# Optimization experiments

Hardware: AMD Instinct MI355X
Metric: run time of the kernel (lower is better)

## Reference

```python
import jax, jax.numpy as jnp
import numpy as np

N, B, PER, NELEM, E = 8192, 32, 256, 5, 131072
H, F, G, L = 128, 128, 50, 6
NC = B * NELEM
CUTOFF = 10.0
LOG2 = float(np.log(2.0))


def ssp(x):
    return jax.nn.softplus(x) - LOG2


def setup_inputs() -> dict:
    key = jax.random.key(0)
    ks = jax.random.split(key, 24)
    pos = jax.random.normal(ks[0], (N, 3), dtype=jnp.float32) * 2.0
    # component structure: node n in graph g gets element slot n % NELEM
    comp_id = (jnp.arange(N) // PER) * NELEM + (jnp.arange(N) % NELEM)
    comps_z = jax.random.randint(ks[1], (NC,), 1, 100)
    z = comps_z[comp_id]
    # edges restricted to within a graph (mimics radius_graph with batch)
    eg = jax.random.randint(ks[2], (E,), 0, B)
    src = eg * PER + jax.random.randint(ks[3], (E,), 0, PER)
    dst = eg * PER + jax.random.randint(ks[4], (E,), 0, PER)
    edge_index = jnp.stack([src, dst], axis=0)
    s = 0.05
    p = lambda k, shp: jax.random.normal(k, shp, dtype=jnp.float32) * s
    return {
        "pos": pos,
        "emb_table": p(ks[5], (100, H)),
        "mlp_w1": p(ks[6], (L, G, F)),
        "mlp_b1": jnp.zeros((L, F), jnp.float32),
        "mlp_w2": p(ks[7], (L, F, F)),
        "mlp_b2": jnp.zeros((L, F), jnp.float32),
        "cf_lin1_w": p(ks[8], (L, H, F)),
        "cf_lin2_w": p(ks[9], (L, F, H)),
        "cf_lin2_b": jnp.zeros((L, H), jnp.float32),
        "int_lin_w": p(ks[10], (L, H, H)),
        "int_lin_b": jnp.zeros((L, H), jnp.float32),
        "out_w1": p(ks[11], (H, H // 2)),
        "out_b1": jnp.zeros((H // 2,), jnp.float32),
        "out_w2": p(ks[12], (H // 2, 1)),
        "out_b2": jnp.zeros((1,), jnp.float32),
        "z": z,
        "comp_id": comp_id,
        "edge_index": edge_index,
        "comps_z": comps_z,
    }


def reference(pos, emb_table, mlp_w1, mlp_b1, mlp_w2, mlp_b2,
              cf_lin1_w, cf_lin2_w, cf_lin2_b, int_lin_w, int_lin_b,
              out_w1, out_b1, out_w2, out_b2,
              z, comp_id, edge_index, comps_z):
    src, dst = edge_index[0], edge_index[1]
    # edge distances and Gaussian smearing
    ew = jnp.linalg.norm(pos[src] - pos[dst], axis=-1)              # [E]
    offset = jnp.linspace(0.0, CUTOFF, G)
    coeff = -0.5 / (offset[1] - offset[0]) ** 2
    edge_attr = jnp.exp(coeff * (ew[:, None] - offset[None, :]) ** 2)  # [E,G]
    # cutoff envelope used by CFConv
    C = CUTOFF / (1e-10 + ew ** 2) - 1.0                            # [E]

    h = emb_table[z]                 # [N,H] node features (fixed across blocks)
    types = emb_table[comps_z]       # [NC,H] component features

    counts = jax.ops.segment_sum(jnp.ones((N,), jnp.float32), comp_id,
                                 num_segments=NC)                   # [NC]
    batch_c = jnp.arange(NC) // NELEM

    for i in range(L):
        # edge filter MLP * cutoff weight
        W = ssp(edge_attr @ mlp_w1[i] + mlp_b1[i]) @ mlp_w2[i] + mlp_b2[i]
        W = W * C[:, None]                                          # [E,F]
        xh = h @ cf_lin1_w[i]                                       # [N,F]
        msg = xh[src] * W                                           # [E,F]
        agg = jax.ops.segment_sum(msg, dst, num_segments=N)         # [N,F]
        # per-component mean pooling
        comp = jax.ops.segment_sum(agg, comp_id, num_segments=NC) / counts[:, None]
        x = comp @ cf_lin2_w[i] + cf_lin2_b[i]                      # [NC,H]
        x = ssp(x) @ int_lin_w[i] + int_lin_b[i]
        types = types + x

    # readout (num_tasks=1, n_seq=None branch)
    h2 = ssp(types @ out_w1 + out_b1)
    per_comp = h2 @ out_w2 + out_b2                                 # [NC,1]
    out = jax.ops.segment_sum(per_comp, batch_c, num_segments=B)    # [B,1]
    return out
```

## Files before the change

kernel.cpp:

```cpp
#include <hip/hip_runtime.h>


#define NNODES 8192
#define NGRAPH 32
#define NELEM  5
#define NEDGE  131072
#define HD     128
#define FD     128
#define GD     50
#define LL     6
#define NC     160
#define NZ     100
#define CUT    10.0f
#define LOG2_  0.69314718055994531f
#define LOG2E_ 1.44269504088896340f
#define QDC    0.84932181f

#define CAP    1024
#define PADE   (NC * CAP)
#define PADG   (PADE / 64)
#define GPITCH 72
#define TPITCH 136
#define CSTR   16

#define W1F_ELEMS (LL * 2 * 8 * 64 * 8)
#define W2F_ELEMS (LL * 4 * 8 * 64 * 8)
#define NSCATB   (NEDGE / 256)
#define NFRAGB   ((W1F_ELEMS + W2F_ELEMS) / 256)
#define NXHZB    (LL * NZ / 2)
#define NB2PB    3

typedef _Float16 half8 __attribute__((ext_vector_type(8)));
typedef float floatx4 __attribute__((ext_vector_type(4)));

#if __has_builtin(__builtin_amdgcn_exp2f)
#define EXP2F(x) __builtin_amdgcn_exp2f(x)
#else
#define EXP2F(x) __expf((x) * LOG2_)
#endif
#if __has_builtin(__builtin_amdgcn_logf)
#define LOG2F_(x) __builtin_amdgcn_logf(x)
#else
#define LOG2F_(x) (__logf(x) * LOG2E_)
#endif

__device__ __forceinline__ float ssp(float x) {
    float m = fmaxf(x, 0.0f);
    float z = __expf(-fabsf(x));
    return m + __logf(1.0f + z) - LOG2_;
}

__global__ __launch_bounds__(256) void setup_kernel(
    const float* __restrict__ pos, const int* __restrict__ ei,
    const int* __restrict__ comp_id, const int* __restrict__ z,
    const float* __restrict__ w1, const float* __restrict__ w2,
    const float* __restrict__ b2in,
    const float* __restrict__ emb, const float* __restrict__ cf1,
    int* __restrict__ counts, int* __restrict__ cursor,
    float* __restrict__ ew_s, float* __restrict__ c_s, int* __restrict__ zsrc_s,
    _Float16* __restrict__ w1f, _Float16* __restrict__ w2f,
    float* __restrict__ xh_z, float* __restrict__ b2p)
{
    int bx = blockIdx.x;
    int tid = threadIdx.x;
    if (bx < NSCATB) {
        int e = bx * 256 + tid;
        int s = ei[e], d = ei[NEDGE + e];
        float dx = pos[3*s]   - pos[3*d];
        float dy = pos[3*s+1] - pos[3*d+1];
        float dz = pos[3*s+2] - pos[3*d+2];
        float d2 = dx*dx + dy*dy + dz*dz;
        float ew = sqrtf(d2);
        float C  = CUT / (1e-10f + d2) - 1.0f;
        int cid = comp_id[d];
        int idx = cid * CAP + atomicAdd(&cursor[cid * CSTR], 1);
        ew_s[idx] = ew; c_s[idx] = C; zsrc_s[idx] = z[s];
        if (e < NNODES) atomicAdd(&counts[comp_id[e]], 1);
        return;
    }
    int fx = bx - NSCATB;
    if (fx < NFRAGB) {
        int idx = fx * 256 + tid;
        if (idx < W1F_ELEMS) {
            int j = idx & 7, lane = (idx >> 3) & 63, tcg = (idx >> 9) & 7;
            int kb = (idx >> 12) & 1, l = idx >> 13;
            int k = kb * 32 + (lane >> 4) * 8 + j;
            int col = tcg * 16 + (lane & 15);
            float v = (k < GD) ? w1[(l * GD + k) * FD + col] : 0.0f;
            w1f[idx] = (_Float16)(v * LOG2E_);
        } else {
            int id2 = idx - W1F_ELEMS;
            int j = id2 & 7, lane = (id2 >> 3) & 63, tcg = (id2 >> 9) & 7;
            int kb = (id2 >> 12) & 3, l = id2 >> 14;
            int k = kb * 32 + (lane >> 4) * 8 + j;
            int col = tcg * 16 + (lane & 15);
            w2f[id2] = (_Float16)(LOG2_ * w2[(l * FD + k) * FD + col]);
        }
        return;
    }
    int bz = fx - NFRAGB;
    if (bz < NXHZB) {
        int l = bz / (NZ / 2);
        int zv = (bz % (NZ / 2)) * 2 + (tid >> 7);
        int f = tid & 127;
        const float* h = emb + zv * HD;
        const float* w = cf1 + l * HD * FD;
        float acc = 0.0f;
        #pragma unroll 8
        for (int k = 0; k < HD; ++k) acc = fmaf(h[k], w[k * FD + f], acc);
        int fp = ((f >> 5) * 32) + ((f & 15) * 2) + ((f >> 4) & 1);
        xh_z[(l * NZ + zv) * FD + fp] = acc;
    } else {
        int idx2 = (bz - NXHZB) * 256 + tid;
        int l = idx2 >> 7, fo = idx2 & 127;
        float sum = 0.0f;
        #pragma unroll 8
        for (int fi = 0; fi < FD; ++fi)
            sum += (float)(_Float16)(LOG2_ * w2[(l * FD + fi) * FD + fo]);
        b2p[idx2] = b2in[l * FD + fo] - sum;
    }
}

__global__ __launch_bounds__(256, 6) void edge_kernel(
    const float* __restrict__ ew_s, const float* __restrict__ c_s,
    const int* __restrict__ zsrc_s,
    const _Float16* __restrict__ w1f, const float* __restrict__ b1_,
    const _Float16* __restrict__ w2f, const float* __restrict__ b2p_,
    const float* __restrict__ xh_z, float* __restrict__ comp_acc)
{
    __shared__ __align__(16) _Float16 smem[64 * TPITCH];
    __shared__ int2 cz_l[64];

    const int tid  = threadIdx.x;
    const int lane = tid & 63;
    const int l15  = lane & 15;
    const int quad = lane >> 4;
    const int fq   = __builtin_amdgcn_readfirstlane(tid >> 6);
    const int cid  = blockIdx.x % NC;
    const int gg   = blockIdx.x / NC;
    const int g0   = cid * CAP + gg * 64;
    const int l0   = blockIdx.y * 3;

    const float ce = c_s[g0 + lane];
    if (__all(ce == 0.0f)) return;
    if (tid < 64)
        cz_l[tid] = make_int2(__float_as_int(ce), zsrc_s[g0 + tid] * (FD * 4));

    const float delta = CUT / (GD - 1);
    const float Qe = QDC / delta;
    half8 ga, gb;
    {
        const float qewr = ew_s[g0 + lane] * Qe;
        #pragma unroll
        for (int i = 0; i < 8; ++i) {
            float u0 = qewr - (fq * 16 + i) * QDC;
            float u1 = qewr - (fq * 16 + 8 + i) * QDC;
            ga[i] = (_Float16)EXP2F(-(u0 * u0));
            gb[i] = (_Float16)EXP2F(-(u1 * u1));
        }
    }
    const int colbase = fq * 32 + l15;
    const int wsw = quad << 4;
    const int rsw = ((l15 >> 2) & 3) << 4;

    #pragma unroll 1
    for (int li = 0; li < 3; ++li) {
        const int l = l0 + li;

        *(half8*)&smem[lane * GPITCH + fq * 16]     = ga;
        *(half8*)&smem[lane * GPITCH + fq * 16 + 8] = gb;
        const float b1c0 = b1_[l * FD + colbase] * LOG2E_;
        const float b1c1 = b1_[l * FD + colbase + 16] * LOG2E_;
        const float b2c0 = b2p_[l * FD + colbase];
        const float b2c1 = b2p_[l * FD + colbase + 16];
        __syncthreads();

        floatx4 accT[4][2];
        #pragma unroll
        for (int tr = 0; tr < 4; ++tr) {
            accT[tr][0] = (floatx4){b1c0, b1c0, b1c0, b1c0};
            accT[tr][1] = (floatx4){b1c1, b1c1, b1c1, b1c1};
        }
        const half8* w1fp = (const half8*)w1f;
        #pragma unroll
        for (int kb = 0; kb < 2; ++kb) {
            half8 bf0 = w1fp[((l * 2 + kb) * 8 + fq * 2 + 0) * 64 + lane];
            half8 bf1 = w1fp[((l * 2 + kb) * 8 + fq * 2 + 1) * 64 + lane];
            #pragma unroll
            for (int tr = 0; tr < 4; ++tr) {
                half8 af = *(const half8*)&smem[(tr * 16 + l15) * GPITCH + kb * 32 + quad * 8];
                accT[tr][0] = __builtin_amdgcn_mfma_f32_16x16x32_f16(af, bf0, accT[tr][0], 0, 0, 0);
                accT[tr][1] = __builtin_amdgcn_mfma_f32_16x16x32_f16(af, bf1, accT[tr][1], 0, 0, 0);
            }
        }
        __syncthreads();

        #pragma unroll
        for (int tr = 0; tr < 4; ++tr) {
            #pragma unroll
            for (int tcl = 0; tcl < 2; ++tcl) {
                #pragma unroll
                for (int r = 0; r < 4; ++r) {
                    float ee = EXP2F(accT[tr][tcl][r]);
                    smem[(tr * 16 + quad * 4 + r) * TPITCH
                         + ((fq * 32 + tcl * 16 + l15) ^ wsw)]
                        = (_Float16)LOG2F_(1.0f + ee);
                }
            }
        }
        __syncthreads();

        floatx4 accW[4][2];
        #pragma unroll
        for (int tr = 0; tr < 4; ++tr) {
            accW[tr][0] = (floatx4){b2c0, b2c0, b2c0, b2c0};
            accW[tr][1] = (floatx4){b2c1, b2c1, b2c1, b2c1};
        }
        const half8* w2fp = (const half8*)w2f;
        #pragma unroll
        for (int kb = 0; kb < 4; ++kb) {
            half8 bf0 = w2fp[((l * 4 + kb) * 8 + fq * 2 + 0) * 64 + lane];
            half8 bf1 = w2fp[((l * 4 + kb) * 8 + fq * 2 + 1) * 64 + lane];
            #pragma unroll
            for (int tr = 0; tr < 4; ++tr) {
                half8 af = *(const half8*)&smem[(tr * 16 + l15) * TPITCH
                                                + ((kb * 32 + quad * 8) ^ rsw)];
                accW[tr][0] = __builtin_amdgcn_mfma_f32_16x16x32_f16(af, bf0, accW[tr][0], 0, 0, 0);
                accW[tr][1] = __builtin_amdgcn_mfma_f32_16x16x32_f16(af, bf1, accW[tr][1], 0, 0, 0);
            }
        }

        const char* xb = (const char*)xh_z
                       + ((size_t)(l * NZ * FD) + (size_t)(fq * 32 + l15 * 2)) * 4;
        float s0 = 0.0f, s1 = 0.0f;
        #pragma unroll
        for (int tr = 0; tr < 4; ++tr) {
            #pragma unroll
            for (int r = 0; r < 4; ++r) {
                const int e = tr * 16 + quad * 4 + r;
                int2 cz = cz_l[e];
                float cee = __int_as_float(cz.x);
                const float2 xr = *(const float2*)(xb + cz.y);
                s0 = fmaf(accW[tr][0][r], cee * xr.x, s0);
                s1 = fmaf(accW[tr][1][r], cee * xr.y, s1);
            }
        }
        s0 += __shfl_xor(s0, 16); s0 += __shfl_xor(s0, 32);
        s1 += __shfl_xor(s1, 16); s1 += __shfl_xor(s1, 32);
        float* cacc = comp_acc + (l * NC + cid) * FD + fq * 32;
        if (quad == 0) {
            atomicAdd(&cacc[l15],      s0);
            atomicAdd(&cacc[l15 + 16], s1);
        }
        if (li < 2) __syncthreads();
    }
}

__global__ __launch_bounds__(128) void comp_kernel(
    const float* __restrict__ comp_acc, const int* __restrict__ counts,
    const float* __restrict__ cf2w, const float* __restrict__ cf2b,
    const float* __restrict__ intw, const float* __restrict__ intb,
    float* __restrict__ types_acc)
{
    int c = blockIdx.x, l = blockIdx.y, f = threadIdx.x;
    __shared__ float comp[FD];
    __shared__ float sx[FD];
    comp[f] = comp_acc[(l * NC + c) * FD + f] / (float)counts[c];
    __syncthreads();
    float acc = cf2b[l * HD + f];
    const float* w = cf2w + l * FD * HD;
    #pragma unroll 8
    for (int k = 0; k < FD; ++k) acc = fmaf(comp[k], w[k * HD + f], acc);
    sx[f] = ssp(acc);
    __syncthreads();
    float acc2 = intb[l * HD + f];
    const float* wi = intw + l * HD * HD;
    #pragma unroll 8
    for (int k = 0; k < HD; ++k) acc2 = fmaf(sx[k], wi[k * HD + f], acc2);
    atomicAdd(&types_acc[c * HD + f], acc2);
}

__global__ __launch_bounds__(64) void readout_kernel(
    const float* __restrict__ types_acc, const float* __restrict__ emb,
    const int* __restrict__ comps_z,
    const float* __restrict__ w1, const float* __restrict__ b1,
    const float* __restrict__ w2, const float* __restrict__ b2,
    float* __restrict__ out)
{
    int b = blockIdx.x, lane = threadIdx.x;
    float sum = 0.0f;
    for (int cc = 0; cc < NELEM; ++cc) {
        int c = b * NELEM + cc;
        int zc = comps_z[c];
        float acc = b1[lane];
        const float* ta = types_acc + c * HD;
        const float* eb = emb + zc * HD;
        #pragma unroll 8
        for (int k = 0; k < HD; ++k) acc = fmaf(ta[k] + eb[k], w1[k * 64 + lane], acc);
        sum += ssp(acc) * w2[lane];
    }
    #pragma unroll
    for (int s = 32; s > 0; s >>= 1) sum += __shfl_xor(sum, s);
    if (lane == 0) out[b] = sum + (float)NELEM * b2[0];
}

extern "C" void kernel_launch(void* const* d_in, const int* in_sizes, int n_in,
                              void* d_out, int out_size, void* d_ws, size_t ws_size,
                              hipStream_t stream) {
    (void)in_sizes; (void)n_in; (void)out_size; (void)ws_size;
    const float* pos     = (const float*)d_in[0];
    const float* emb     = (const float*)d_in[1];
    const float* mlp_w1  = (const float*)d_in[2];
    const float* mlp_b1  = (const float*)d_in[3];
    const float* mlp_w2  = (const float*)d_in[4];
    const float* mlp_b2  = (const float*)d_in[5];
    const float* cf1     = (const float*)d_in[6];
    const float* cf2w    = (const float*)d_in[7];
    const float* cf2b    = (const float*)d_in[8];
    const float* intw    = (const float*)d_in[9];
    const float* intb    = (const float*)d_in[10];
    const float* ow1     = (const float*)d_in[11];
    const float* ob1     = (const float*)d_in[12];
    const float* ow2     = (const float*)d_in[13];
    const float* ob2     = (const float*)d_in[14];
    const int*   z       = (const int*)d_in[15];
    const int*   comp_id = (const int*)d_in[16];
    const int*   ei      = (const int*)d_in[17];
    const int*   comps_z = (const int*)d_in[18];
    float* out = (float*)d_out;

    char* ws = (char*)d_ws;
    size_t off = 0;
    auto alloc = [&](size_t bytes) -> void* {
        void* p = ws + off;
        off += (bytes + 255) & ~(size_t)255;
        return p;
    };
    float* comp_acc  = (float*)alloc((size_t)LL * NC * FD * 4);
    int*   counts    = (int*)  alloc(NC * 4);
    float* types_acc = (float*)alloc((size_t)NC * HD * 4);
    int*   cursor    = (int*)  alloc(NC * CSTR * 4);
    float* c_s       = (float*)alloc((size_t)PADE * 4);
    int*   zsrc_s    = (int*)  alloc((size_t)PADE * 4);
    float* ew_s      = (float*)alloc((size_t)PADE * 4);
    size_t zero_bytes = off;
    float* xh_z     = (float*)alloc((size_t)LL * NZ * FD * 4);
    float* b2p      = (float*)alloc((size_t)LL * FD * 4);
    _Float16* w1f   = (_Float16*)alloc((size_t)W1F_ELEMS * 2);
    _Float16* w2f   = (_Float16*)alloc((size_t)W2F_ELEMS * 2);

    hipMemsetAsync(d_ws, 0, zero_bytes, stream);

    setup_kernel<<<NSCATB + NFRAGB + NXHZB + NB2PB, 256, 0, stream>>>(
        pos, ei, comp_id, z, mlp_w1, mlp_w2, mlp_b2, emb, cf1,
        counts, cursor, ew_s, c_s, zsrc_s, w1f, w2f, xh_z, b2p);
    edge_kernel <<<dim3(PADG, 2), 256, 0, stream>>>(ew_s, c_s, zsrc_s,
                                                    w1f, mlp_b1, w2f, b2p,
                                                    xh_z, comp_acc);
    comp_kernel <<<dim3(NC, LL), 128, 0, stream>>>(comp_acc, counts, cf2w, cf2b,
                                                   intw, intb, types_acc);
    readout_kernel<<<NGRAPH, 64, 0, stream>>>(types_acc, emb, comps_z,
                                              ow1, ob1, ow2, ob2, out);
}
```

Before: 224.7 us.

## Launch one edge block per layer and pack softplus writes with permuted W2 fragments

Result: faster. 214.8 us (-4.4%).

```diff
diff --git a/kernel.cpp b/kernel.cpp
--- a/kernel.cpp
+++ b/kernel.cpp
@@ -31,6 +31,7 @@
 #define NB2PB    3
 
 typedef _Float16 half8 __attribute__((ext_vector_type(8)));
+typedef __fp16 fp16x2 __attribute__((ext_vector_type(2)));
 typedef float floatx4 __attribute__((ext_vector_type(4)));
 
 #if __has_builtin(__builtin_amdgcn_exp2f)
@@ -92,7 +93,8 @@
             int id2 = idx - W1F_ELEMS;
             int j = id2 & 7, lane = (id2 >> 3) & 63, tcg = (id2 >> 9) & 7;
             int kb = (id2 >> 12) & 3, l = id2 >> 14;
-            int k = kb * 32 + (lane >> 4) * 8 + j;
+            int kf = (lane >> 4) * 8 + j;
+            int k = kb * 32 + ((kf & 1) << 4) + (kf >> 1);
             int col = tcg * 16 + (lane & 15);
             w2f[id2] = (_Float16)(LOG2_ * w2[(l * FD + k) * FD + col]);
         }
@@ -121,7 +123,7 @@
     }
 }
 
-__global__ __launch_bounds__(256, 6) void edge_kernel(
+__global__ __launch_bounds__(256, 8) void edge_kernel(
     const float* __restrict__ ew_s, const float* __restrict__ c_s,
     const int* __restrict__ zsrc_s,
     const _Float16* __restrict__ w1f, const float* __restrict__ b1_,
@@ -136,21 +138,28 @@
     const int l15  = lane & 15;
     const int quad = lane >> 4;
     const int fq   = __builtin_amdgcn_readfirstlane(tid >> 6);
+    const int l    = blockIdx.y;
     const int cid  = blockIdx.x % NC;
     const int gg   = blockIdx.x / NC;
     const int g0   = cid * CAP + gg * 64;
-    const int l0   = blockIdx.y * 3;
+
+    const float delta = CUT / (GD - 1);
+    const float Qe = QDC / delta;
 
     const float ce = c_s[g0 + lane];
     if (__all(ce == 0.0f)) return;
     if (tid < 64)
         cz_l[tid] = make_int2(__float_as_int(ce), zsrc_s[g0 + tid] * (FD * 4));
 
-    const float delta = CUT / (GD - 1);
-    const float Qe = QDC / delta;
-    half8 ga, gb;
+    const int colbase = fq * 32 + l15;
+    const float b1c0 = b1_[l * FD + colbase] * LOG2E_;
+    const float b1c1 = b1_[l * FD + colbase + 16] * LOG2E_;
+    const float b2c0 = b2p_[l * FD + colbase];
+    const float b2c1 = b2p_[l * FD + colbase + 16];
+
     {
         const float qewr = ew_s[g0 + lane] * Qe;
+        half8 ga, gb;
         #pragma unroll
         for (int i = 0; i < 8; ++i) {
             float u0 = qewr - (fq * 16 + i) * QDC;
@@ -158,101 +167,89 @@
             ga[i] = (_Float16)EXP2F(-(u0 * u0));
             gb[i] = (_Float16)EXP2F(-(u1 * u1));
         }
-    }
-    const int colbase = fq * 32 + l15;
-    const int wsw = quad << 4;
-    const int rsw = ((l15 >> 2) & 3) << 4;
-
-    #pragma unroll 1
-    for (int li = 0; li < 3; ++li) {
-        const int l = l0 + li;
-
         *(half8*)&smem[lane * GPITCH + fq * 16]     = ga;
         *(half8*)&smem[lane * GPITCH + fq * 16 + 8] = gb;
-        const float b1c0 = b1_[l * FD + colbase] * LOG2E_;
-        const float b1c1 = b1_[l * FD + colbase + 16] * LOG2E_;
-        const float b2c0 = b2p_[l * FD + colbase];
-        const float b2c1 = b2p_[l * FD + colbase + 16];
-        __syncthreads();
-
-        floatx4 accT[4][2];
+    }
+    __syncthreads();
+
+    floatx4 accT[4][2];
+    #pragma unroll
+    for (int tr = 0; tr < 4; ++tr) {
+        accT[tr][0] = (floatx4){b1c0, b1c0, b1c0, b1c0};
+        accT[tr][1] = (floatx4){b1c1, b1c1, b1c1, b1c1};
+    }
+    const half8* w1fp = (const half8*)w1f;
+    #pragma unroll
+    for (int kb = 0; kb < 2; ++kb) {
+        half8 bf0 = w1fp[((l * 2 + kb) * 8 + fq * 2 + 0) * 64 + lane];
+        half8 bf1 = w1fp[((l * 2 + kb) * 8 + fq * 2 + 1) * 64 + lane];
         #pragma unroll
         for (int tr = 0; tr < 4; ++tr) {
-            accT[tr][0] = (floatx4){b1c0, b1c0, b1c0, b1c0};
-            accT[tr][1] = (floatx4){b1c1, b1c1, b1c1, b1c1};
-        }
-        const half8* w1fp = (const half8*)w1f;
-        #pragma unroll
-        for (int kb = 0; kb < 2; ++kb) {
-            half8 bf0 = w1fp[((l * 2 + kb) * 8 + fq * 2 + 0) * 64 + lane];
-            half8 bf1 = w1fp[((l * 2 + kb) * 8 + fq * 2 + 1) * 64 + lane];
-            #pragma unroll
-            for (int tr = 0; tr < 4; ++tr) {
-                half8 af = *(const half8*)&smem[(tr * 16 + l15) * GPITCH + kb * 32 + quad * 8];
-                accT[tr][0] = __builtin_amdgcn_mfma_f32_16x16x32_f16(af, bf0, accT[tr][0], 0, 0, 0);
-                accT[tr][1] = __builtin_amdgcn_mfma_f32_16x16x32_f16(af, bf1, accT[tr][1], 0, 0, 0);
-            }
-        }
-        __syncthreads();
-
+            half8 af = *(const half8*)&smem[(tr * 16 + l15) * GPITCH + kb * 32 + quad * 8];
+            accT[tr][0] = __builtin_amdgcn_mfma_f32_16x16x32_f16(af, bf0, accT[tr][0], 0, 0, 0);
+            accT[tr][1] = __builtin_amdgcn_mfma_f32_16x16x32_f16(af, bf1, accT[tr][1], 0, 0, 0);
+        }
+    }
+    __syncthreads();
+
+    #pragma unroll
+    for (int tr = 0; tr < 4; ++tr) {
+        #pragma unroll
+        for (int r = 0; r < 4; ++r) {
+            float e0 = EXP2F(accT[tr][0][r]);
+            float e1 = EXP2F(accT[tr][1][r]);
+            float s0f = LOG2F_(1.0f + e0);
+            float s1f = LOG2F_(1.0f + e1);
+#if __has_builtin(__builtin_amdgcn_cvt_pkrtz)
+            fp16x2 pk = __builtin_amdgcn_cvt_pkrtz(s0f, s1f);
+#else
+            fp16x2 pk; pk[0] = (__fp16)s0f; pk[1] = (__fp16)s1f;
+#endif
+            *(fp16x2*)&smem[(tr * 16 + quad * 4 + r) * TPITCH + fq * 32 + l15 * 2] = pk;
+        }
+    }
+    __syncthreads();
+
+    floatx4 accW[4][2];
+    #pragma unroll
+    for (int tr = 0; tr < 4; ++tr) {
+        accW[tr][0] = (floatx4){b2c0, b2c0, b2c0, b2c0};
+        accW[tr][1] = (floatx4){b2c1, b2c1, b2c1, b2c1};
+    }
+    const half8* w2fp = (const half8*)w2f;
+    #pragma unroll
+    for (int kb = 0; kb < 4; ++kb) {
+        half8 bf0 = w2fp[((l * 4 + kb) * 8 + fq * 2 + 0) * 64 + lane];
+        half8 bf1 = w2fp[((l * 4 + kb) * 8 + fq * 2 + 1) * 64 + lane];
         #pragma unroll
         for (int tr = 0; tr < 4; ++tr) {
-            #pragma unroll
-            for (int tcl = 0; tcl < 2; ++tcl) {
-                #pragma unroll
-                for (int r = 0; r < 4; ++r) {
-                    float ee = EXP2F(accT[tr][tcl][r]);
-                    smem[(tr * 16 + quad * 4 + r) * TPITCH
-                         + ((fq * 32 + tcl * 16 + l15) ^ wsw)]
-                        = (_Float16)LOG2F_(1.0f + ee);
-                }
-            }
-        }
-        __syncthreads();
-
-        floatx4 accW[4][2];
-        #pragma unroll
-        for (int tr = 0; tr < 4; ++tr) {
-            accW[tr][0] = (floatx4){b2c0, b2c0, b2c0, b2c0};
-            accW[tr][1] = (floatx4){b2c1, b2c1, b2c1, b2c1};
-        }
-        const half8* w2fp = (const half8*)w2f;
-        #pragma unroll
-        for (int kb = 0; kb < 4; ++kb) {
-            half8 bf0 = w2fp[((l * 4 + kb) * 8 + fq * 2 + 0) * 64 + lane];
-            half8 bf1 = w2fp[((l * 4 + kb) * 8 + fq * 2 + 1) * 64 + lane];
-            #pragma unroll
-            for (int tr = 0; tr < 4; ++tr) {
-                half8 af = *(const half8*)&smem[(tr * 16 + l15) * TPITCH
-                                                + ((kb * 32 + quad * 8) ^ rsw)];
-                accW[tr][0] = __builtin_amdgcn_mfma_f32_16x16x32_f16(af, bf0, accW[tr][0], 0, 0, 0);
-                accW[tr][1] = __builtin_amdgcn_mfma_f32_16x16x32_f16(af, bf1, accW[tr][1], 0, 0, 0);
-            }
-        }
-
-        const char* xb = (const char*)xh_z
-                       + ((size_t)(l * NZ * FD) + (size_t)(fq * 32 + l15 * 2)) * 4;
-        float s0 = 0.0f, s1 = 0.0f;
-        #pragma unroll
-        for (int tr = 0; tr < 4; ++tr) {
-            #pragma unroll
-            for (int r = 0; r < 4; ++r) {
-                const int e = tr * 16 + quad * 4 + r;
-                int2 cz = cz_l[e];
-                float cee = __int_as_float(cz.x);
-                const float2 xr = *(const float2*)(xb + cz.y);
-                s0 = fmaf(accW[tr][0][r], cee * xr.x, s0);
-                s1 = fmaf(accW[tr][1][r], cee * xr.y, s1);
-            }
-        }
-        s0 += __shfl_xor(s0, 16); s0 += __shfl_xor(s0, 32);
-        s1 += __shfl_xor(s1, 16); s1 += __shfl_xor(s1, 32);
-        float* cacc = comp_acc + (l * NC + cid) * FD + fq * 32;
-        if (quad == 0) {
-            atomicAdd(&cacc[l15],      s0);
-            atomicAdd(&cacc[l15 + 16], s1);
-        }
-        if (li < 2) __syncthreads();
+            half8 af = *(const half8*)&smem[(tr * 16 + l15) * TPITCH + kb * 32 + quad * 8];
+            accW[tr][0] = __builtin_amdgcn_mfma_f32_16x16x32_f16(af, bf0, accW[tr][0], 0, 0, 0);
+            accW[tr][1] = __builtin_amdgcn_mfma_f32_16x16x32_f16(af, bf1, accW[tr][1], 0, 0, 0);
+        }
+    }
+
+    const char* xb = (const char*)xh_z
+                   + ((size_t)(l * NZ * FD) + (size_t)(fq * 32 + l15 * 2)) * 4;
+    float s0 = 0.0f, s1 = 0.0f;
+    #pragma unroll
+    for (int tr = 0; tr < 4; ++tr) {
+        #pragma unroll
+        for (int r = 0; r < 4; ++r) {
+            const int e = tr * 16 + quad * 4 + r;
+            int2 cz = cz_l[e];
+            float cee = __int_as_float(cz.x);
+            const float2 xr = *(const float2*)(xb + cz.y);
+            s0 = fmaf(accW[tr][0][r], cee * xr.x, s0);
+            s1 = fmaf(accW[tr][1][r], cee * xr.y, s1);
+        }
+    }
+    s0 += __shfl_xor(s0, 16); s0 += __shfl_xor(s0, 32);
+    s1 += __shfl_xor(s1, 16); s1 += __shfl_xor(s1, 32);
+    float* cacc = comp_acc + (l * NC + cid) * FD + fq * 32;
+    if (quad == 0) {
+        atomicAdd(&cacc[l15],      s0);
+        atomicAdd(&cacc[l15 + 16], s1);
     }
 }
 
@@ -349,14 +346,14 @@
     _Float16* w1f   = (_Float16*)alloc((size_t)W1F_ELEMS * 2);
     _Float16* w2f   = (_Float16*)alloc((size_t)W2F_ELEMS * 2);
 
-    hipMemsetAsync(d_ws, 0, zero_bytes, stream);
+    (void)hipMemsetAsync(d_ws, 0, zero_bytes, stream);
 
     setup_kernel<<<NSCATB + NFRAGB + NXHZB + NB2PB, 256, 0, stream>>>(
         pos, ei, comp_id, z, mlp_w1, mlp_w2, mlp_b2, emb, cf1,
         counts, cursor, ew_s, c_s, zsrc_s, w1f, w2f, xh_z, b2p);
-    edge_kernel <<<dim3(PADG, 2), 256, 0, stream>>>(ew_s, c_s, zsrc_s,
-                                                    w1f, mlp_b1, w2f, b2p,
-                                                    xh_z, comp_acc);
+    edge_kernel <<<dim3(PADG, LL), 256, 0, stream>>>(ew_s, c_s, zsrc_s,
+                                                     w1f, mlp_b1, w2f, b2p,
+                                                     xh_z, comp_acc);
     comp_kernel <<<dim3(NC, LL), 128, 0, stream>>>(comp_acc, counts, cf2w, cf2b,
                                                    intw, intb, types_acc);
     readout_kernel<<<NGRAPH, 64, 0, stream>>>(types_acc, emb, comps_z,
```
